# Optimization experiments

Hardware: AMD Instinct MI355X
Metric: run time of the kernel (lower is better)

The kernel has to match this reference:

```python
import jax, jax.numpy as jnp
import numpy as np

jax.config.update("jax_enable_x64", True)  # original module computes in torch.float64

NUM_CLASSES = 6625
FEAT_DIM = 96
CLAMP_MIN = 1e-12
CLAMP_MAX = 1e12


def setup_inputs() -> dict:
    key = jax.random.key(0)
    k1, k2, k3 = jax.random.split(key, 3)
    features = jax.random.normal(k1, (64, 64, FEAT_DIM), dtype=jnp.float32)   # [B, T, D]
    predicts = jax.random.normal(k2, (64, 64, NUM_CLASSES), dtype=jnp.float32)  # [B, T, C] logits
    centers = jax.random.normal(k3, (NUM_CLASSES, FEAT_DIM), dtype=jnp.float32)  # learned centers
    return {"features": features, "predicts": predicts, "centers": centers}


def reference(features, predicts, centers):
    # Flatten [B, T, D] -> [N, D], cast to float64 as the torch module does.
    feats = features.reshape(-1, features.shape[-1]).astype(jnp.float64)  # [N, D]
    label = jnp.argmax(predicts, axis=2).reshape(-1)                      # [N] int
    cen = centers.astype(jnp.float64)                                     # [C, D]
    n = feats.shape[0]
    c = cen.shape[0]

    sq_feat = jnp.sum(feats * feats, axis=1, keepdims=True)               # [N, 1]
    sq_center = jnp.sum(cen * cen, axis=1)                                # [C]
    distmat = sq_feat + sq_center[None, :] - 2.0 * (feats @ cen.T)        # [N, C]

    # Keep only the column matching each sample's label, clamp, sum, normalize by N.
    mask = (jnp.arange(c)[None, :] == label[:, None]).astype(jnp.float64)  # [N, C]
    dist = distmat * mask
    loss = jnp.sum(jnp.clip(dist, CLAMP_MIN, CLAMP_MAX)) / n
    return loss
```

## Files before the change

### kernel.cpp

```cpp
#include <hip/hip_runtime.h>

#define NUM_CLASSES 6625
#define FEAT_DIM 96
#define NROWS 4096
#define CLAMP_MIN 1e-12
#define CLAMP_MAX 1e12

__global__ __launch_bounds__(256) void argmax_dist_kernel(
    const float* __restrict__ pred,
    const float* __restrict__ feats,
    const float* __restrict__ centers,
    double* __restrict__ dists)
{
    const int C = NUM_CLASSES;
    const int row = blockIdx.x;
    const int tid = threadIdx.x;
    const float* p = pred + (size_t)row * C;

    const int prefix = (4 - (row & 3)) & 3;
    const int nvec = (C - prefix) >> 2;
    const float4* pv = (const float4*)(p + prefix);

    float4 v0 = pv[tid];
    float4 v1 = pv[tid + 256];
    float4 v2 = pv[tid + 512];
    float4 v3 = pv[tid + 768];
    float4 v4 = pv[tid + 1024];
    float4 v5 = pv[tid + 1280];
    const int i6 = tid + 1536;
    const bool val6 = i6 < nvec;
    float4 v6 = pv[val6 ? i6 : (nvec - 1)];
    const bool valp = tid < prefix;
    float vp = p[valp ? tid : 0];
    const int tailstart = prefix + 4 * nvec;
    const bool valt = tid < (C - tailstart);
    float vt = p[valt ? (tailstart + tid) : 0];

    float b0, b1, b2, b3, b4, b5, b6;
    int   j0, j1, j2, j3, j4, j5, j6;
    b0=b1=b2=b3=b4=b5=b6 = -__builtin_inff();
    j0=j1=j2=j3=j4=j5=j6 = C;

    if (valp) { b0 = vp; j0 = tid; }

    #define CHAIN(vv, bb, jj, vecidx) { \
        const int e = prefix + 4 * (vecidx); \
        if (vv.x > bb) { bb = vv.x; jj = e; } \
        if (vv.y > bb) { bb = vv.y; jj = e + 1; } \
        if (vv.z > bb) { bb = vv.z; jj = e + 2; } \
        if (vv.w > bb) { bb = vv.w; jj = e + 3; } }
    CHAIN(v0, b0, j0, tid)
    CHAIN(v1, b1, j1, tid + 256)
    CHAIN(v2, b2, j2, tid + 512)
    CHAIN(v3, b3, j3, tid + 768)
    CHAIN(v4, b4, j4, tid + 1024)
    CHAIN(v5, b5, j5, tid + 1280)
    if (val6) CHAIN(v6, b6, j6, i6)
    #undef CHAIN
    if (valt) {
        const int e = tailstart + tid;
        if (vt > b6) { b6 = vt; j6 = e; }
    }

    float best = b0; int bidx = j0;
    #define MERGE(bb, jj) if (bb > best || (bb == best && jj < bidx)) { best = bb; bidx = jj; }
    MERGE(b1, j1) MERGE(b2, j2) MERGE(b3, j3)
    MERGE(b4, j4) MERGE(b5, j5) MERGE(b6, j6)
    #undef MERGE

    for (int off = 32; off > 0; off >>= 1) {
        float ov = __shfl_down(best, off, 64);
        int   oi = __shfl_down(bidx, off, 64);
        if (ov > best || (ov == best && oi < bidx)) { best = ov; bidx = oi; }
    }

    __shared__ float swv[4];
    __shared__ int   swi[4];
    const int wave = tid >> 6;
    const int lane = tid & 63;
    if (lane == 0) { swv[wave] = best; swi[wave] = bidx; }
    __syncthreads();
    if (tid >= 64) return;

    float bv = swv[0]; int bi = swi[0];
    #pragma unroll
    for (int w = 1; w < 4; ++w) {
        float v2 = swv[w]; int i2 = swi[w];
        if (v2 > bv || (v2 == bv && i2 < bi)) { bv = v2; bi = i2; }
    }
    const int label = bi;

    const float* frow = feats + row * FEAT_DIM;
    const float* crow = centers + (size_t)label * FEAT_DIM;
    double d0 = (double)frow[lane] - (double)crow[lane];
    double acc = d0 * d0;
    if (lane < 32) {
        double d1 = (double)frow[lane + 64] - (double)crow[lane + 64];
        acc += d1 * d1;
    }
    for (int off = 32; off > 0; off >>= 1)
        acc += __shfl_down(acc, off, 64);
    if (lane == 0) {
        double dn = acc;
        dn = dn < CLAMP_MIN ? CLAMP_MIN : (dn > CLAMP_MAX ? CLAMP_MAX : dn);
        dists[row] = dn;
    }
}

__global__ __launch_bounds__(256) void reduce_kernel(
    const double* __restrict__ dists, float* __restrict__ out)
{
    const int tid = threadIdx.x;
    double s = 0.0;
    #pragma unroll
    for (int i = 0; i < NROWS / 256; ++i) s += dists[tid + i * 256];
    for (int off = 32; off > 0; off >>= 1)
        s += __shfl_down(s, off, 64);
    __shared__ double sw[4];
    const int wave = tid >> 6;
    const int lane = tid & 63;
    if (lane == 0) sw[wave] = s;
    __syncthreads();
    if (tid == 0) {
        double t = sw[0] + sw[1] + sw[2] + sw[3];
        out[0] = (float)(t / (double)NROWS
                         + (double)(NUM_CLASSES - 1) * CLAMP_MIN);
    }
}

extern "C" void kernel_launch(void* const* d_in, const int* in_sizes, int n_in,
                              void* d_out, int out_size, void* d_ws, size_t ws_size,
                              hipStream_t stream) {
    const float* feats   = (const float*)d_in[0];
    const float* pred    = (const float*)d_in[1];
    const float* centers = (const float*)d_in[2];
    double* dists = (double*)d_ws;
    float* out = (float*)d_out;

    argmax_dist_kernel<<<NROWS, 256, 0, stream>>>(pred, feats, centers, dists);
    reduce_kernel<<<1, 256, 0, stream>>>(dists, out);
}
```

Baseline: 25.40 us.

## Assign one wavefront per row for argmax instead of one block per row

Each 64-lane wavefront now handles a whole prediction row, and each block covers four rows, so the grid shrinks by four. Each lane streams about 26 float4 values in three unrolled batches of eight loads instead of 7 loads spread over 256 threads. This drops the shared-memory cross-wave reduction and the __syncthreads, and the idle waves that sat out the distance step, in exchange for longer per-lane serial chains and more registers held per lane.

```diff
diff --git a/kernel.cpp b/kernel.cpp
--- a/kernel.cpp
+++ b/kernel.cpp
@@ -13,35 +13,20 @@
     double* __restrict__ dists)
 {
     const int C = NUM_CLASSES;
-    const int row = blockIdx.x;
-    const int tid = threadIdx.x;
+    const int lane = threadIdx.x & 63;
+    const int row  = blockIdx.x * 4 + (threadIdx.x >> 6);
     const float* p = pred + (size_t)row * C;
 
     const int prefix = (4 - (row & 3)) & 3;
     const int nvec = (C - prefix) >> 2;
     const float4* pv = (const float4*)(p + prefix);
 
-    float4 v0 = pv[tid];
-    float4 v1 = pv[tid + 256];
-    float4 v2 = pv[tid + 512];
-    float4 v3 = pv[tid + 768];
-    float4 v4 = pv[tid + 1024];
-    float4 v5 = pv[tid + 1280];
-    const int i6 = tid + 1536;
-    const bool val6 = i6 < nvec;
-    float4 v6 = pv[val6 ? i6 : (nvec - 1)];
-    const bool valp = tid < prefix;
-    float vp = p[valp ? tid : 0];
-    const int tailstart = prefix + 4 * nvec;
-    const bool valt = tid < (C - tailstart);
-    float vt = p[valt ? (tailstart + tid) : 0];
+    float b0, b1, b2, b3, b4, b5, b6, b7;
+    int   j0, j1, j2, j3, j4, j5, j6, j7;
+    b0=b1=b2=b3=b4=b5=b6=b7 = -__builtin_inff();
+    j0=j1=j2=j3=j4=j5=j6=j7 = C;
 
-    float b0, b1, b2, b3, b4, b5, b6;
-    int   j0, j1, j2, j3, j4, j5, j6;
-    b0=b1=b2=b3=b4=b5=b6 = -__builtin_inff();
-    j0=j1=j2=j3=j4=j5=j6 = C;
-
-    if (valp) { b0 = vp; j0 = tid; }
+    if (lane < prefix) { b0 = p[lane]; j0 = lane; }
 
     #define CHAIN(vv, bb, jj, vecidx) { \
         const int e = prefix + 4 * (vecidx); \
@@ -49,23 +34,51 @@
         if (vv.y > bb) { bb = vv.y; jj = e + 1; } \
         if (vv.z > bb) { bb = vv.z; jj = e + 2; } \
         if (vv.w > bb) { bb = vv.w; jj = e + 3; } }
-    CHAIN(v0, b0, j0, tid)
-    CHAIN(v1, b1, j1, tid + 256)
-    CHAIN(v2, b2, j2, tid + 512)
-    CHAIN(v3, b3, j3, tid + 768)
-    CHAIN(v4, b4, j4, tid + 1024)
-    CHAIN(v5, b5, j5, tid + 1280)
-    if (val6) CHAIN(v6, b6, j6, i6)
+
+    #pragma unroll
+    for (int bat = 0; bat < 3; ++bat) {
+        const int base = lane + 512 * bat;
+        float4 w0 = pv[base];
+        float4 w1 = pv[base +  64];
+        float4 w2 = pv[base + 128];
+        float4 w3 = pv[base + 192];
+        float4 w4 = pv[base + 256];
+        float4 w5 = pv[base + 320];
+        float4 w6 = pv[base + 384];
+        float4 w7 = pv[base + 448];
+        CHAIN(w0, b0, j0, base)
+        CHAIN(w1, b1, j1, base +  64)
+        CHAIN(w2, b2, j2, base + 128)
+        CHAIN(w3, b3, j3, base + 192)
+        CHAIN(w4, b4, j4, base + 256)
+        CHAIN(w5, b5, j5, base + 320)
+        CHAIN(w6, b6, j6, base + 384)
+        CHAIN(w7, b7, j7, base + 448)
+    }
+    {
+        const int i24 = lane + 1536;
+        float4 w0 = pv[i24];
+        const int i25 = lane + 1600;
+        const bool v25 = i25 < nvec;
+        float4 w1 = pv[v25 ? i25 : (nvec - 1)];
+        CHAIN(w0, b0, j0, i24)
+        if (v25) CHAIN(w1, b1, j1, i25)
+    }
     #undef CHAIN
-    if (valt) {
-        const int e = tailstart + tid;
-        if (vt > b6) { b6 = vt; j6 = e; }
+
+    {
+        const int tailstart = prefix + 4 * nvec;
+        const int tails = C - tailstart;
+        if (lane < tails) {
+            const float v = p[tailstart + lane];
+            if (v > b7) { b7 = v; j7 = tailstart + lane; }
+        }
     }
 
     float best = b0; int bidx = j0;
     #define MERGE(bb, jj) if (bb > best || (bb == best && jj < bidx)) { best = bb; bidx = jj; }
     MERGE(b1, j1) MERGE(b2, j2) MERGE(b3, j3)
-    MERGE(b4, j4) MERGE(b5, j5) MERGE(b6, j6)
+    MERGE(b4, j4) MERGE(b5, j5) MERGE(b6, j6) MERGE(b7, j7)
     #undef MERGE
 
     for (int off = 32; off > 0; off >>= 1) {
@@ -73,22 +86,7 @@
         int   oi = __shfl_down(bidx, off, 64);
         if (ov > best || (ov == best && oi < bidx)) { best = ov; bidx = oi; }
     }
-
-    __shared__ float swv[4];
-    __shared__ int   swi[4];
-    const int wave = tid >> 6;
-    const int lane = tid & 63;
-    if (lane == 0) { swv[wave] = best; swi[wave] = bidx; }
-    __syncthreads();
-    if (tid >= 64) return;
-
-    float bv = swv[0]; int bi = swi[0];
-    #pragma unroll
-    for (int w = 1; w < 4; ++w) {
-        float v2 = swv[w]; int i2 = swi[w];
-        if (v2 > bv || (v2 == bv && i2 < bi)) { bv = v2; bi = i2; }
-    }
-    const int label = bi;
+    const int label = __shfl(bidx, 0, 64);
 
     const float* frow = feats + row * FEAT_DIM;
     const float* crow = centers + (size_t)label * FEAT_DIM;
@@ -137,6 +135,6 @@
     double* dists = (double*)d_ws;
     float* out = (float*)d_out;
 
-    argmax_dist_kernel<<<NROWS, 256, 0, stream>>>(pred, feats, centers, dists);
+    argmax_dist_kernel<<<NROWS / 4, 256, 0, stream>>>(pred, feats, centers, dists);
     reduce_kernel<<<1, 256, 0, stream>>>(dists, out);
 }
```

Result: slower. 26.39 us (+3.9%).
